# Optimization experiments

Hardware: AMD Instinct MI355X
Metric: run time of the kernel (lower is better)

The kernel has to match this reference:

```python
import jax, jax.numpy as jnp
import numpy as np

H = 512  # hidden_dim

def setup_inputs() -> dict:
    key = jax.random.key(0)
    k1, k2, k3, k4, k5 = jax.random.split(key, 5)
    B, S = 32, 2048
    hidden = jax.random.normal(k1, (B, 2 * H), dtype=jnp.float32)
    encoder_outputs = jax.random.normal(k2, (B, S, 2 * H), dtype=jnp.float32)
    # nn.Linear(4H, H): weight [H, 4H], bias [H]
    W = jax.random.normal(k3, (H, 4 * H), dtype=jnp.float32) / np.sqrt(4 * H)
    b = jnp.zeros((H,), dtype=jnp.float32)
    v = jax.random.normal(k4, (H,), dtype=jnp.float32) / np.sqrt(H)
    return {"hidden": hidden, "encoder_outputs": encoder_outputs, "W": W, "b": b, "v": v}

def reference(hidden, encoder_outputs, W, b, v):
    B, S, _ = encoder_outputs.shape
    # concat repeated decoder hidden with encoder outputs: [B, S, 4H]
    hidden_rep = jnp.broadcast_to(hidden[:, None, :], (B, S, hidden.shape[-1]))
    cat = jnp.concatenate([hidden_rep, encoder_outputs], axis=-1)
    energy = jnp.tanh(jnp.einsum('bsf,hf->bsh', cat, W) + b)  # [B, S, H]
    scores = jnp.einsum('bsh,h->bs', energy, v)               # [B, S]
    attn = jax.nn.softmax(scores, axis=1)                     # softmax over seq
    context = jnp.einsum('bsd,bs->bd', encoder_outputs, attn) # [B, 2H]
    return context
```

## Files before the change

kernel.cpp:

```cpp
#include <hip/hip_runtime.h>


typedef __attribute__((ext_vector_type(8))) short short8;
typedef __attribute__((ext_vector_type(4))) short short4v;
typedef __attribute__((ext_vector_type(4))) float f4;

__device__ __forceinline__ unsigned short bf16_rn(float x) {
    unsigned int u = __float_as_uint(x);
    return (unsigned short)((u + 0x7FFFu + ((u >> 16) & 1u)) >> 16);
}
__device__ __forceinline__ float bf16_to_f(unsigned short h) {
    return __uint_as_float(((unsigned int)h) << 16);
}
__device__ __forceinline__ void gload_lds16(const void* g, void* l) {
    __builtin_amdgcn_global_load_lds(
        (const __attribute__((address_space(1))) unsigned int*)g,
        (__attribute__((address_space(3))) unsigned int*)l, 16, 0, 0);
}

__global__ __launch_bounds__(256) void prep_kernel(
    const float* __restrict__ hidden, const float* __restrict__ W,
    const float* __restrict__ bias, float* __restrict__ u,
    unsigned short* __restrict__ w2hi, unsigned short* __restrict__ w2lo) {
    if (blockIdx.x < 64) {
        int t = blockIdx.x * 256 + threadIdx.x;
        int b = t >> 9, h = t & 511;
        const f4* wr = (const f4*)(W + (size_t)h * 2048);
        const f4* hr = (const f4*)(hidden + (size_t)b * 1024);
        float acc = bias[h];
        #pragma unroll 4
        for (int i = 0; i < 256; ++i) {
            f4 w4 = wr[i]; f4 h4 = hr[i];
            acc += w4[0]*h4[0] + w4[1]*h4[1] + w4[2]*h4[2] + w4[3]*h4[3];
        }
        u[t] = acc;
    } else {
        int g = (blockIdx.x - 64) * 256 + threadIdx.x;
        int kk = g >> 11, id = g & 2047;
        int nt = id >> 6, q = (id >> 4) & 3, c = id & 15;
        int h = nt * 16 + c;
        const float* src = W + (size_t)h * 2048 + 1024 + kk * 32 + q * 8;
        short8 vhi, vlo;
        #pragma unroll
        for (int j = 0; j < 8; ++j) {
            float x = src[j];
            unsigned short hb = bf16_rn(x);
            unsigned short lb = bf16_rn(x - bf16_to_f(hb));
            vhi[j] = (short)hb; vlo[j] = (short)lb;
        }
        ((short8*)w2hi)[g] = vhi;
        ((short8*)w2lo)[g] = vlo;
    }
}

__global__ __launch_bounds__(512, 6) void score_kernel(
    const float* __restrict__ enc, const unsigned short* __restrict__ w2hi,
    const unsigned short* __restrict__ w2lo, const float* __restrict__ u,
    const float* __restrict__ v, float* __restrict__ scores_part) {
    __shared__ short Ahi[2048], Alo[2048];
    __shared__ short Bhi[8192], Blo[8192];
    __shared__ float u_s[256], v_s[256];
    __shared__ float partial[8][64];

    const int tid  = threadIdx.x;
    const int wl   = tid >> 6, lane = tid & 63;
    const int q    = lane >> 4, m = lane & 15;
    const int sblk = blockIdx.x >> 1, hh = blockIdx.x & 1;
    const int row0 = sblk * 64;
    const int b    = row0 >> 11;
    const float* encB = enc + (size_t)row0 * 1024;

    if (tid < 256) {
        u_s[tid] = u[(b << 9) + (hh << 8) + tid];
        v_s[tid] = v[(hh << 8) + tid];
    }

    f4 acc[4][2];
    #pragma unroll
    for (int mt = 0; mt < 4; ++mt)
        #pragma unroll
        for (int nt = 0; nt < 2; ++nt) acc[mt][nt] = (f4){0.f, 0.f, 0.f, 0.f};

    const int c8   = tid >> 1, half = tid & 1;
    const int arow = ((c8 >> 6) << 4) + (c8 & 15);
    const int akof = (((c8 >> 4) & 3) << 3) + (half << 2);
    const float* aBase = encB + (size_t)arow * 1024 + akof;

    for (int kk = 0; kk < 32; ++kk) {
        __syncthreads();
        {
            f4 x = *(const f4*)(aBase + (kk << 5));
            short4v vhi, vlo;
            #pragma unroll
            for (int j = 0; j < 4; ++j) {
                unsigned short hb = bf16_rn(x[j]);
                vhi[j] = (short)hb; vlo[j] = (short)bf16_rn(x[j] - bf16_to_f(hb));
            }
            ((short4v*)Ahi)[tid] = vhi;
            ((short4v*)Alo)[tid] = vlo;
        }
        {
            const size_t srcOff = (size_t)kk * 32768 + (hh << 14) + (wl << 11) + lane * 16;
            #pragma unroll
            for (int i = 0; i < 2; ++i) {
                unsigned int off = (unsigned int)((wl << 11) + (i << 10));
                gload_lds16((const char*)w2hi + srcOff + (i << 10), (char*)Bhi + off);
                gload_lds16((const char*)w2lo + srcOff + (i << 10), (char*)Blo + off);
            }
        }
        __syncthreads();
        short8 ah[4], al[4];
        #pragma unroll
        for (int mt = 0; mt < 4; ++mt) {
            int idx = (mt << 6) + (q << 4) + m;
            ah[mt] = ((short8*)Ahi)[idx];
            al[mt] = ((short8*)Alo)[idx];
        }
        #pragma unroll
        for (int nt = 0; nt < 2; ++nt) {
            int ntl = (wl << 1) + nt;
            int bidx = (ntl << 6) + (q << 4) + m;
            short8 bh = ((short8*)Bhi)[bidx];
            short8 bl = ((short8*)Blo)[bidx];
            #pragma unroll
            for (int mt = 0; mt < 4; ++mt) {
                acc[mt][nt] = __builtin_amdgcn_mfma_f32_16x16x32_bf16(ah[mt], bh, acc[mt][nt], 0, 0, 0);
                acc[mt][nt] = __builtin_amdgcn_mfma_f32_16x16x32_bf16(ah[mt], bl, acc[mt][nt], 0, 0, 0);
                acc[mt][nt] = __builtin_amdgcn_mfma_f32_16x16x32_bf16(al[mt], bh, acc[mt][nt], 0, 0, 0);
            }
        }
    }
    #pragma unroll
    for (int mt = 0; mt < 4; ++mt) {
        #pragma unroll
        for (int reg = 0; reg < 4; ++reg) {
            float ssum = 0.f;
            #pragma unroll
            for (int nt = 0; nt < 2; ++nt) {
                int hl = (wl << 5) + (nt << 4) + m;
                float e = tanhf(u_s[hl] + acc[mt][nt][reg]);
                ssum += v_s[hl] * e;
            }
            ssum += __shfl_xor(ssum, 1);
            ssum += __shfl_xor(ssum, 2);
            ssum += __shfl_xor(ssum, 4);
            ssum += __shfl_xor(ssum, 8);
            if (m == 0) partial[wl][(mt << 4) + (q << 2) + reg] = ssum;
        }
    }
    __syncthreads();
    if (tid < 64) {
        float s = 0.f;
        #pragma unroll
        for (int w = 0; w < 8; ++w) s += partial[w][tid];
        scores_part[(hh << 16) + row0 + tid] = s;
    }
}

__global__ __launch_bounds__(256) void ctx_partial_kernel(
    const float* __restrict__ enc, const float* __restrict__ scores_part,
    float* __restrict__ partials) {
    __shared__ float p_s[2048];
    __shared__ float wredm[4], wreds[4];
    const int t = threadIdx.x;
    const int b = blockIdx.x >> 5, sc = blockIdx.x & 31;
    const int wid = t >> 6, lane = t & 63;
    const float* s0 = scores_part + ((size_t)b << 11);
    const float* s1 = s0 + 65536;

    float vals[8];
    float mx = -1e30f;
    #pragma unroll
    for (int i = 0; i < 8; ++i) {
        int idx = t + (i << 8);
        vals[i] = s0[idx] + s1[idx];
        mx = fmaxf(mx, vals[i]);
    }
    #pragma unroll
    for (int off = 1; off < 64; off <<= 1) mx = fmaxf(mx, __shfl_xor(mx, off));
    if (lane == 0) wredm[wid] = mx;
    __syncthreads();
    mx = fmaxf(fmaxf(wredm[0], wredm[1]), fmaxf(wredm[2], wredm[3]));

    float lsum = 0.f;
    #pragma unroll
    for (int i = 0; i < 8; ++i) {
        float e = __expf(vals[i] - mx);
        p_s[t + (i << 8)] = e;
        lsum += e;
    }
    #pragma unroll
    for (int off = 1; off < 64; off <<= 1) lsum += __shfl_xor(lsum, off);
    if (lane == 0) wreds[wid] = lsum;
    __syncthreads();
    const float inv = 1.f / (wreds[0] + wreds[1] + wreds[2] + wreds[3]);

    f4 a = (f4){0.f, 0.f, 0.f, 0.f};
    const f4* erow = ((const f4*)(enc + ((size_t)b * 2048 + (sc << 6)) * 1024)) + t;
    #pragma unroll 4
    for (int i = 0; i < 64; ++i) {
        float p = p_s[(sc << 6) + i] * inv;
        f4 e = erow[(size_t)i << 8];
        a += p * e;
    }
    f4* dst = (f4*)(partials + (((size_t)(sc << 5) + b) << 10));
    dst[t] = a;
}

__global__ __launch_bounds__(256) void ctx_reduce_kernel(
    const float* __restrict__ partials, float* __restrict__ out) {
    int i = blockIdx.x * 256 + threadIdx.x;
    float s = 0.f;
    #pragma unroll
    for (int sc = 0; sc < 32; ++sc) s += partials[sc * 32768 + i];
    out[i] = s;
}

extern "C" void kernel_launch(void* const* d_in, const int* in_sizes, int n_in,
                              void* d_out, int out_size, void* d_ws, size_t ws_size,
                              hipStream_t stream) {
    const float* hidden = (const float*)d_in[0];
    const float* enc    = (const float*)d_in[1];
    const float* W      = (const float*)d_in[2];
    const float* bias   = (const float*)d_in[3];
    const float* v      = (const float*)d_in[4];
    float* out = (float*)d_out;
    char* ws = (char*)d_ws;

    float* u              = (float*)(ws);
    float* scores_part    = (float*)(ws + 65536);
    float* partials       = (float*)(ws + 589824);
    unsigned short* w2hi  = (unsigned short*)(ws + 4784128);
    unsigned short* w2lo  = (unsigned short*)(ws + 5832704);

    prep_kernel<<<320, 256, 0, stream>>>(hidden, W, bias, u, w2hi, w2lo);
    score_kernel<<<2048, 512, 0, stream>>>(enc, w2hi, w2lo, u, v, scores_part);
    ctx_partial_kernel<<<1024, 256, 0, stream>>>(enc, scores_part, partials);
    ctx_reduce_kernel<<<128, 256, 0, stream>>>(partials, out);
}
```

Measured before the change: 592.3 us.

## Double score tile rows to reuse B tiles and use truncating bf16 split

The score kernel block now covers 128 sequence rows instead of 64, and each wave computes a 4x4 MFMA tile (64 rows by 64 hidden) instead of 4x2. The staged W tile is therefore reused across twice as many rows, which halves the B-tile global/LDS traffic per row and the grid size. The fp32-to-bf16 hi/lo split of the activations now uses a byte-permute truncation instead of round-to-nearest, which needs fewer ALU ops. In exchange there is higher register pressure (occupancy hint lowered to 4) and slightly less accurate hi/lo splitting.

```diff
diff --git a/kernel.cpp b/kernel.cpp
--- a/kernel.cpp
+++ b/kernel.cpp
@@ -2,8 +2,8 @@
 
 
 typedef __attribute__((ext_vector_type(8))) short short8;
-typedef __attribute__((ext_vector_type(4))) short short4v;
 typedef __attribute__((ext_vector_type(4))) float f4;
+typedef __attribute__((ext_vector_type(4))) unsigned int uint4v;
 
 __device__ __forceinline__ unsigned short bf16_rn(float x) {
     unsigned int u = __float_as_uint(x);
@@ -11,6 +11,12 @@
 }
 __device__ __forceinline__ float bf16_to_f(unsigned short h) {
     return __uint_as_float(((unsigned int)h) << 16);
+}
+__device__ __forceinline__ unsigned int pack2_trunc(float a, float b) {
+    return __builtin_amdgcn_perm(__float_as_uint(b), __float_as_uint(a), 0x07060302u);
+}
+__device__ __forceinline__ float trunc_hi(float x) {
+    return __uint_as_float(__float_as_uint(x) & 0xFFFF0000u);
 }
 __device__ __forceinline__ void gload_lds16(const void* g, void* l) {
     __builtin_amdgcn_global_load_lds(
@@ -53,20 +59,21 @@
     }
 }
 
-__global__ __launch_bounds__(512, 6) void score_kernel(
+__global__ __launch_bounds__(512, 4) void score_kernel(
     const float* __restrict__ enc, const unsigned short* __restrict__ w2hi,
     const unsigned short* __restrict__ w2lo, const float* __restrict__ u,
     const float* __restrict__ v, float* __restrict__ scores_part) {
-    __shared__ short Ahi[2048], Alo[2048];
+    __shared__ short Ahi[4096], Alo[4096];
     __shared__ short Bhi[8192], Blo[8192];
     __shared__ float u_s[256], v_s[256];
-    __shared__ float partial[8][64];
+    __shared__ float partial[4][128];
 
     const int tid  = threadIdx.x;
     const int wl   = tid >> 6, lane = tid & 63;
     const int q    = lane >> 4, m = lane & 15;
+    const int half = wl >> 2, nq = wl & 3;
     const int sblk = blockIdx.x >> 1, hh = blockIdx.x & 1;
-    const int row0 = sblk * 64;
+    const int row0 = sblk * 128;
     const int b    = row0 >> 11;
     const float* encB = enc + (size_t)row0 * 1024;
 
@@ -75,29 +82,32 @@
         v_s[tid] = v[(hh << 8) + tid];
     }
 
-    f4 acc[4][2];
+    f4 acc[4][4];
     #pragma unroll
     for (int mt = 0; mt < 4; ++mt)
         #pragma unroll
-        for (int nt = 0; nt < 2; ++nt) acc[mt][nt] = (f4){0.f, 0.f, 0.f, 0.f};
-
-    const int c8   = tid >> 1, half = tid & 1;
-    const int arow = ((c8 >> 6) << 4) + (c8 & 15);
-    const int akof = (((c8 >> 4) & 3) << 3) + (half << 2);
+        for (int nt = 0; nt < 4; ++nt) acc[mt][nt] = (f4){0.f, 0.f, 0.f, 0.f};
+
+    const int arow = ((tid >> 6) << 4) + (tid & 15);
+    const int akof = ((tid >> 4) & 3) << 3;
     const float* aBase = encB + (size_t)arow * 1024 + akof;
 
     for (int kk = 0; kk < 32; ++kk) {
         __syncthreads();
         {
-            f4 x = *(const f4*)(aBase + (kk << 5));
-            short4v vhi, vlo;
-            #pragma unroll
-            for (int j = 0; j < 4; ++j) {
-                unsigned short hb = bf16_rn(x[j]);
-                vhi[j] = (short)hb; vlo[j] = (short)bf16_rn(x[j] - bf16_to_f(hb));
-            }
-            ((short4v*)Ahi)[tid] = vhi;
-            ((short4v*)Alo)[tid] = vlo;
+            f4 x0 = *(const f4*)(aBase + (kk << 5));
+            f4 x1 = *(const f4*)(aBase + (kk << 5) + 4);
+            uint4v hp, lp;
+            hp[0] = pack2_trunc(x0[0], x0[1]);
+            hp[1] = pack2_trunc(x0[2], x0[3]);
+            hp[2] = pack2_trunc(x1[0], x1[1]);
+            hp[3] = pack2_trunc(x1[2], x1[3]);
+            lp[0] = pack2_trunc(x0[0] - trunc_hi(x0[0]), x0[1] - trunc_hi(x0[1]));
+            lp[1] = pack2_trunc(x0[2] - trunc_hi(x0[2]), x0[3] - trunc_hi(x0[3]));
+            lp[2] = pack2_trunc(x1[0] - trunc_hi(x1[0]), x1[1] - trunc_hi(x1[1]));
+            lp[3] = pack2_trunc(x1[2] - trunc_hi(x1[2]), x1[3] - trunc_hi(x1[3]));
+            ((uint4v*)Ahi)[tid] = hp;
+            ((uint4v*)Alo)[tid] = lp;
         }
         {
             const size_t srcOff = (size_t)kk * 32768 + (hh << 14) + (wl << 11) + lane * 16;
@@ -112,14 +122,14 @@
         short8 ah[4], al[4];
         #pragma unroll
         for (int mt = 0; mt < 4; ++mt) {
-            int idx = (mt << 6) + (q << 4) + m;
+            int idx = ((((half << 2) + mt) << 2) + q) * 16 + m;
             ah[mt] = ((short8*)Ahi)[idx];
             al[mt] = ((short8*)Alo)[idx];
         }
         #pragma unroll
-        for (int nt = 0; nt < 2; ++nt) {
-            int ntl = (wl << 1) + nt;
-            int bidx = (ntl << 6) + (q << 4) + m;
+        for (int nt = 0; nt < 4; ++nt) {
+            int ntg = (nq << 2) + nt;
+            int bidx = ((ntg << 2) + q) * 16 + m;
             short8 bh = ((short8*)Bhi)[bidx];
             short8 bl = ((short8*)Blo)[bidx];
             #pragma unroll
@@ -136,8 +146,8 @@
         for (int reg = 0; reg < 4; ++reg) {
             float ssum = 0.f;
             #pragma unroll
-            for (int nt = 0; nt < 2; ++nt) {
-                int hl = (wl << 5) + (nt << 4) + m;
+            for (int nt = 0; nt < 4; ++nt) {
+                int hl = (nq << 6) + (nt << 4) + m;
                 float e = tanhf(u_s[hl] + acc[mt][nt][reg]);
                 ssum += v_s[hl] * e;
             }
@@ -145,14 +155,12 @@
             ssum += __shfl_xor(ssum, 2);
             ssum += __shfl_xor(ssum, 4);
             ssum += __shfl_xor(ssum, 8);
-            if (m == 0) partial[wl][(mt << 4) + (q << 2) + reg] = ssum;
+            if (m == 0) partial[nq][(half << 6) + (mt << 4) + (q << 2) + reg] = ssum;
         }
     }
     __syncthreads();
-    if (tid < 64) {
-        float s = 0.f;
-        #pragma unroll
-        for (int w = 0; w < 8; ++w) s += partial[w][tid];
+    if (tid < 128) {
+        float s = partial[0][tid] + partial[1][tid] + partial[2][tid] + partial[3][tid];
         scores_part[(hh << 16) + row0 + tid] = s;
     }
 }
@@ -234,7 +242,7 @@
     unsigned short* w2lo  = (unsigned short*)(ws + 5832704);
 
     prep_kernel<<<320, 256, 0, stream>>>(hidden, W, bias, u, w2hi, w2lo);
-    score_kernel<<<2048, 512, 0, stream>>>(enc, w2hi, w2lo, u, v, scores_part);
+    score_kernel<<<1024, 512, 0, stream>>>(enc, w2hi, w2lo, u, v, scores_part);
     ctx_partial_kernel<<<1024, 256, 0, stream>>>(enc, scores_part, partials);
     ctx_reduce_kernel<<<128, 256, 0, stream>>>(partials, out);
 }
```

Measured after the change: 635.2 us. 1.07x slower.

## Switch score GEMM to fp16 two-term split with 32x32 MFMA tiles

Applied to the files above, without the earlier changes.

Replaces the three-product bf16 hi/lo emulation with fp16 MFMA. The encoder operand is split into fp16 hi+lo, while the weights get a single fp16 copy, so each step needs two MFMAs instead of three. It also moves from 16x16x32 to 32x32x16 tiles with 256-thread blocks, halves the weight staging traffic, and swaps tanhf for an exp-based formula. This cuts matrix-core work and LDS/global traffic, but truncating the weights to fp16 and using round-toward-zero conversion plus the fast exp lowers accuracy.

```diff
diff --git a/kernel.cpp b/kernel.cpp
--- a/kernel.cpp
+++ b/kernel.cpp
@@ -1,27 +1,25 @@
 #include <hip/hip_runtime.h>
 
 
-typedef __attribute__((ext_vector_type(8))) short short8;
-typedef __attribute__((ext_vector_type(4))) short short4v;
-typedef __attribute__((ext_vector_type(4))) float f4;
-
-__device__ __forceinline__ unsigned short bf16_rn(float x) {
-    unsigned int u = __float_as_uint(x);
-    return (unsigned short)((u + 0x7FFFu + ((u >> 16) & 1u)) >> 16);
-}
-__device__ __forceinline__ float bf16_to_f(unsigned short h) {
-    return __uint_as_float(((unsigned int)h) << 16);
-}
+typedef __fp16   half2v __attribute__((ext_vector_type(2)));
+typedef _Float16 half8  __attribute__((ext_vector_type(8)));
+typedef __attribute__((ext_vector_type(4)))  float f4;
+typedef __attribute__((ext_vector_type(16))) float f16v;
+typedef __attribute__((ext_vector_type(4)))  unsigned int uint4v;
+
 __device__ __forceinline__ void gload_lds16(const void* g, void* l) {
     __builtin_amdgcn_global_load_lds(
         (const __attribute__((address_space(1))) unsigned int*)g,
         (__attribute__((address_space(3))) unsigned int*)l, 16, 0, 0);
 }
+__device__ __forceinline__ unsigned int bc2(half2v h) {
+    return __builtin_bit_cast(unsigned int, h);
+}
 
 __global__ __launch_bounds__(256) void prep_kernel(
     const float* __restrict__ hidden, const float* __restrict__ W,
     const float* __restrict__ bias, float* __restrict__ u,
-    unsigned short* __restrict__ w2hi, unsigned short* __restrict__ w2lo) {
+    unsigned short* __restrict__ w2) {
     if (blockIdx.x < 64) {
         int t = blockIdx.x * 256 + threadIdx.x;
         int b = t >> 9, h = t & 511;
@@ -37,122 +35,128 @@
     } else {
         int g = (blockIdx.x - 64) * 256 + threadIdx.x;
         int kk = g >> 11, id = g & 2047;
-        int nt = id >> 6, q = (id >> 4) & 3, c = id & 15;
-        int h = nt * 16 + c;
-        const float* src = W + (size_t)h * 2048 + 1024 + kk * 32 + q * 8;
-        short8 vhi, vlo;
-        #pragma unroll
-        for (int j = 0; j < 8; ++j) {
-            float x = src[j];
-            unsigned short hb = bf16_rn(x);
-            unsigned short lb = bf16_rn(x - bf16_to_f(hb));
-            vhi[j] = (short)hb; vlo[j] = (short)lb;
-        }
-        ((short8*)w2hi)[g] = vhi;
-        ((short8*)w2lo)[g] = vlo;
-    }
-}
-
-__global__ __launch_bounds__(512, 6) void score_kernel(
-    const float* __restrict__ enc, const unsigned short* __restrict__ w2hi,
-    const unsigned short* __restrict__ w2lo, const float* __restrict__ u,
-    const float* __restrict__ v, float* __restrict__ scores_part) {
+        int ntg = id >> 7, kh = (id >> 6) & 1, l = id & 63;
+        int h = (ntg << 5) + (l & 31);
+        int kg = 1024 + (kk << 5) + (kh << 4) + ((l >> 5) << 3);
+        const float* src = W + (size_t)h * 2048 + kg;
+        f4 x0 = *(const f4*)src;
+        f4 x1 = *(const f4*)(src + 4);
+        half8 vh;
+        #pragma unroll
+        for (int j = 0; j < 4; ++j) vh[j] = (_Float16)x0[j];
+        #pragma unroll
+        for (int j = 0; j < 4; ++j) vh[4 + j] = (_Float16)x1[j];
+        ((half8*)w2)[g] = vh;
+    }
+}
+
+__global__ __launch_bounds__(256, 3) void score_kernel(
+    const float* __restrict__ enc, const unsigned short* __restrict__ w2,
+    const float* __restrict__ u, const float* __restrict__ v,
+    float* __restrict__ scores_part) {
     __shared__ short Ahi[2048], Alo[2048];
-    __shared__ short Bhi[8192], Blo[8192];
+    __shared__ short Bs[8192];
     __shared__ float u_s[256], v_s[256];
-    __shared__ float partial[8][64];
+    __shared__ float partial[4][64];
 
     const int tid  = threadIdx.x;
     const int wl   = tid >> 6, lane = tid & 63;
-    const int q    = lane >> 4, m = lane & 15;
+    const int col  = lane & 31;
     const int sblk = blockIdx.x >> 1, hh = blockIdx.x & 1;
     const int row0 = sblk * 64;
     const int b    = row0 >> 11;
     const float* encB = enc + (size_t)row0 * 1024;
 
-    if (tid < 256) {
-        u_s[tid] = u[(b << 9) + (hh << 8) + tid];
-        v_s[tid] = v[(hh << 8) + tid];
-    }
-
-    f4 acc[4][2];
-    #pragma unroll
-    for (int mt = 0; mt < 4; ++mt)
-        #pragma unroll
-        for (int nt = 0; nt < 2; ++nt) acc[mt][nt] = (f4){0.f, 0.f, 0.f, 0.f};
-
-    const int c8   = tid >> 1, half = tid & 1;
-    const int arow = ((c8 >> 6) << 4) + (c8 & 15);
-    const int akof = (((c8 >> 4) & 3) << 3) + (half << 2);
-    const float* aBase = encB + (size_t)arow * 1024 + akof;
+    u_s[tid] = u[(b << 9) + (hh << 8) + tid];
+    v_s[tid] = v[(hh << 8) + tid];
+
+    f16v acc[2][2];
+    #pragma unroll
+    for (int mt = 0; mt < 2; ++mt)
+        #pragma unroll
+        for (int nt = 0; nt < 2; ++nt)
+            #pragma unroll
+            for (int r = 0; r < 16; ++r) acc[mt][nt][r] = 0.f;
+
+    const int s_mt = tid >> 7, s_kh = (tid >> 6) & 1, s_l = tid & 63;
+    const int s_row = (s_mt << 5) + (s_l & 31);
+    const int s_kb  = (s_kh << 4) + ((s_l >> 5) << 3);
+    const float* aSrc = encB + (size_t)s_row * 1024 + s_kb;
+
+    const half8* Ah8 = (const half8*)Ahi;
+    const half8* Al8 = (const half8*)Alo;
+    const half8* Bh8 = (const half8*)Bs;
 
     for (int kk = 0; kk < 32; ++kk) {
+        f4 x0 = *(const f4*)(aSrc + (kk << 5));
+        f4 x1 = *(const f4*)(aSrc + (kk << 5) + 4);
         __syncthreads();
         {
-            f4 x = *(const f4*)(aBase + (kk << 5));
-            short4v vhi, vlo;
-            #pragma unroll
-            for (int j = 0; j < 4; ++j) {
-                unsigned short hb = bf16_rn(x[j]);
-                vhi[j] = (short)hb; vlo[j] = (short)bf16_rn(x[j] - bf16_to_f(hb));
+            half2v h01 = __builtin_amdgcn_cvt_pkrtz(x0[0], x0[1]);
+            half2v h23 = __builtin_amdgcn_cvt_pkrtz(x0[2], x0[3]);
+            half2v h45 = __builtin_amdgcn_cvt_pkrtz(x1[0], x1[1]);
+            half2v h67 = __builtin_amdgcn_cvt_pkrtz(x1[2], x1[3]);
+            half2v l01 = __builtin_amdgcn_cvt_pkrtz(x0[0] - (float)h01[0], x0[1] - (float)h01[1]);
+            half2v l23 = __builtin_amdgcn_cvt_pkrtz(x0[2] - (float)h23[0], x0[3] - (float)h23[1]);
+            half2v l45 = __builtin_amdgcn_cvt_pkrtz(x1[0] - (float)h45[0], x1[1] - (float)h45[1]);
+            half2v l67 = __builtin_amdgcn_cvt_pkrtz(x1[2] - (float)h67[0], x1[3] - (float)h67[1]);
+            uint4v hp = {bc2(h01), bc2(h23), bc2(h45), bc2(h67)};
+            uint4v lp = {bc2(l01), bc2(l23), bc2(l45), bc2(l67)};
+            ((uint4v*)Ahi)[tid] = hp;
+            ((uint4v*)Alo)[tid] = lp;
+        }
+        {
+            const char* bsrc = (const char*)w2 + (size_t)kk * 32768 + (hh << 14)
+                               + (wl << 12) + lane * 16;
+            char* bdst = (char*)Bs + (wl << 12);
+            #pragma unroll
+            for (int i = 0; i < 4; ++i)
+                gload_lds16(bsrc + (i << 10), bdst + (i << 10));
+        }
+        __syncthreads();
+        #pragma unroll
+        for (int kh = 0; kh < 2; ++kh) {
+            half8 ah0 = Ah8[(kh << 6) + lane];
+            half8 ah1 = Ah8[128 + (kh << 6) + lane];
+            half8 al0 = Al8[(kh << 6) + lane];
+            half8 al1 = Al8[128 + (kh << 6) + lane];
+            #pragma unroll
+            for (int nt = 0; nt < 2; ++nt) {
+                int ntl = (wl << 1) + nt;
+                half8 b8 = Bh8[((ntl << 1) + kh) * 64 + lane];
+                acc[0][nt] = __builtin_amdgcn_mfma_f32_32x32x16_f16(ah0, b8, acc[0][nt], 0, 0, 0);
+                acc[0][nt] = __builtin_amdgcn_mfma_f32_32x32x16_f16(al0, b8, acc[0][nt], 0, 0, 0);
+                acc[1][nt] = __builtin_amdgcn_mfma_f32_32x32x16_f16(ah1, b8, acc[1][nt], 0, 0, 0);
+                acc[1][nt] = __builtin_amdgcn_mfma_f32_32x32x16_f16(al1, b8, acc[1][nt], 0, 0, 0);
             }
-            ((short4v*)Ahi)[tid] = vhi;
-            ((short4v*)Alo)[tid] = vlo;
-        }
-        {
-            const size_t srcOff = (size_t)kk * 32768 + (hh << 14) + (wl << 11) + lane * 16;
-            #pragma unroll
-            for (int i = 0; i < 2; ++i) {
-                unsigned int off = (unsigned int)((wl << 11) + (i << 10));
-                gload_lds16((const char*)w2hi + srcOff + (i << 10), (char*)Bhi + off);
-                gload_lds16((const char*)w2lo + srcOff + (i << 10), (char*)Blo + off);
-            }
-        }
-        __syncthreads();
-        short8 ah[4], al[4];
-        #pragma unroll
-        for (int mt = 0; mt < 4; ++mt) {
-            int idx = (mt << 6) + (q << 4) + m;
-            ah[mt] = ((short8*)Ahi)[idx];
-            al[mt] = ((short8*)Alo)[idx];
-        }
-        #pragma unroll
-        for (int nt = 0; nt < 2; ++nt) {
-            int ntl = (wl << 1) + nt;
-            int bidx = (ntl << 6) + (q << 4) + m;
-            short8 bh = ((short8*)Bhi)[bidx];
-            short8 bl = ((short8*)Blo)[bidx];
-            #pragma unroll
-            for (int mt = 0; mt < 4; ++mt) {
-                acc[mt][nt] = __builtin_amdgcn_mfma_f32_16x16x32_bf16(ah[mt], bh, acc[mt][nt], 0, 0, 0);
-                acc[mt][nt] = __builtin_amdgcn_mfma_f32_16x16x32_bf16(ah[mt], bl, acc[mt][nt], 0, 0, 0);
-                acc[mt][nt] = __builtin_amdgcn_mfma_f32_16x16x32_bf16(al[mt], bh, acc[mt][nt], 0, 0, 0);
-            }
-        }
-    }
-    #pragma unroll
-    for (int mt = 0; mt < 4; ++mt) {
-        #pragma unroll
-        for (int reg = 0; reg < 4; ++reg) {
+        }
+    }
+    const int rhalf = (lane >> 5) << 2;
+    #pragma unroll
+    for (int mt = 0; mt < 2; ++mt) {
+        #pragma unroll
+        for (int reg = 0; reg < 16; ++reg) {
             float ssum = 0.f;
             #pragma unroll
             for (int nt = 0; nt < 2; ++nt) {
-                int hl = (wl << 5) + (nt << 4) + m;
-                float e = tanhf(u_s[hl] + acc[mt][nt][reg]);
-                ssum += v_s[hl] * e;
+                int hl = (((wl << 1) + nt) << 5) + col;
+                float x = u_s[hl] + acc[mt][nt][reg];
+                float t = __expf(2.f * x);
+                float th = 1.f - 2.f / (t + 1.f);
+                ssum += v_s[hl] * th;
             }
             ssum += __shfl_xor(ssum, 1);
             ssum += __shfl_xor(ssum, 2);
             ssum += __shfl_xor(ssum, 4);
             ssum += __shfl_xor(ssum, 8);
-            if (m == 0) partial[wl][(mt << 4) + (q << 2) + reg] = ssum;
+            ssum += __shfl_xor(ssum, 16);
+            if (col == 0)
+                partial[wl][(mt << 5) + (reg & 3) + ((reg >> 2) << 3) + rhalf] = ssum;
         }
     }
     __syncthreads();
     if (tid < 64) {
-        float s = 0.f;
-        #pragma unroll
-        for (int w = 0; w < 8; ++w) s += partial[w][tid];
+        float s = partial[0][tid] + partial[1][tid] + partial[2][tid] + partial[3][tid];
         scores_part[(hh << 16) + row0 + tid] = s;
     }
 }
@@ -227,14 +231,13 @@
     float* out = (float*)d_out;
     char* ws = (char*)d_ws;
 
-    float* u              = (float*)(ws);
-    float* scores_part    = (float*)(ws + 65536);
-    float* partials       = (float*)(ws + 589824);
-    unsigned short* w2hi  = (unsigned short*)(ws + 4784128);
-    unsigned short* w2lo  = (unsigned short*)(ws + 5832704);
-
-    prep_kernel<<<320, 256, 0, stream>>>(hidden, W, bias, u, w2hi, w2lo);
-    score_kernel<<<2048, 512, 0, stream>>>(enc, w2hi, w2lo, u, v, scores_part);
+    float* u            = (float*)(ws);
+    float* scores_part  = (float*)(ws + 65536);
+    float* partials     = (float*)(ws + 589824);
+    unsigned short* w2  = (unsigned short*)(ws + 4784128);
+
+    prep_kernel<<<320, 256, 0, stream>>>(hidden, W, bias, u, w2);
+    score_kernel<<<2048, 256, 0, stream>>>(enc, w2, u, v, scores_part);
     ctx_partial_kernel<<<1024, 256, 0, stream>>>(enc, scores_part, partials);
     ctx_reduce_kernel<<<128, 256, 0, stream>>>(partials, out);
 }
```

Result: faster. 548.7 us (-7.4%).
